# Kernel tuning notes

Measured on AMD Instinct MI355X. Metric: run time of the kernel, lower is better.

The kernel has to match this reference:

```python
import jax, jax.numpy as jnp
import numpy as np
from jax import lax

TWN_THRESHOLD_FACTOR = 0.05
BN_EPS = 1e-5


@jax.custom_vjp
def _ternary_quant(w, t):
    return (w > t).astype(w.dtype) - (w < -t).astype(w.dtype)

def _tq_fwd(w, t):
    mask = (w > t) | (w < -t)
    return _ternary_quant(w, t), mask

def _tq_bwd(mask, g):
    return (g * mask.astype(g.dtype), jnp.zeros((), g.dtype))

_ternary_quant.defvjp(_tq_fwd, _tq_bwd)


def quantize(w):
    # threshold is detached in the original (weight.detach().abs().max())
    t = TWN_THRESHOLD_FACTOR * jnp.max(jnp.abs(lax.stop_gradient(w)))
    return _ternary_quant(w, t)


def conv2d(x, w, b):
    # x: [N,C,H,W], w: [O,I,K,K], valid conv, stride 1
    y = lax.conv_general_dilated(x, w, (1, 1), 'VALID',
                                 dimension_numbers=('NCHW', 'OIHW', 'NCHW'))
    return y + b[None, :, None, None]


def maxpool2(x):
    return lax.reduce_window(x, -jnp.inf, lax.max,
                             (1, 1, 2, 2), (1, 1, 2, 2), 'VALID')


def bn2d(x, g, b):
    # training-mode batch norm over (N,H,W), biased variance
    m = jnp.mean(x, (0, 2, 3), keepdims=True)
    v = jnp.mean(jnp.square(x - m), (0, 2, 3), keepdims=True)
    return (x - m) * lax.rsqrt(v + BN_EPS) * g[None, :, None, None] + b[None, :, None, None]


def bn1d(x, g, b):
    m = jnp.mean(x, 0, keepdims=True)
    v = jnp.mean(jnp.square(x - m), 0, keepdims=True)
    return (x - m) * lax.rsqrt(v + BN_EPS) * g[None, :] + b[None, :]


def setup_inputs() -> dict:
    key = jax.random.key(0)
    ks = jax.random.split(key, 12)
    N = 4096
    inp = {
        'x': jax.random.normal(ks[0], (N, 1, 28, 28), jnp.float32),
        'w1': jax.random.normal(ks[1], (32, 1, 5, 5), jnp.float32) * 0.2,
        'b1': jnp.zeros((32,), jnp.float32),
        'g1': jnp.ones((32,), jnp.float32),
        'be1': jnp.zeros((32,), jnp.float32),
        'w2': jax.random.normal(ks[2], (64, 32, 5, 5), jnp.float32) * 0.05,
        'b2': jnp.zeros((64,), jnp.float32),
        'g2': jnp.ones((64,), jnp.float32),
        'be2': jnp.zeros((64,), jnp.float32),
        'wf1': jax.random.normal(ks[3], (512, 1024), jnp.float32) * 0.03,
        'bf1': jnp.zeros((512,), jnp.float32),
        'g3': jnp.ones((512,), jnp.float32),
        'be3': jnp.zeros((512,), jnp.float32),
        'wf2': jax.random.normal(ks[4], (10, 512), jnp.float32) * 0.04,
        'bf2': jnp.zeros((10,), jnp.float32),
    }
    return inp


def reference(x, w1, b1, g1, be1, w2, b2, g2, be2, wf1, bf1, g3, be3, wf2, bf2):
    h = jax.nn.relu(bn2d(conv2d(x, quantize(w1), b1), g1, be1))     # [N,32,24,24]
    h = maxpool2(h)                                                  # [N,32,12,12]
    h = jax.nn.relu(bn2d(conv2d(h, quantize(w2), b2), g2, be2))     # [N,64,8,8]
    h = maxpool2(h)                                                  # [N,64,4,4]
    h = h.reshape(h.shape[0], -1)                                    # [N,1024]
    h = jax.nn.relu(bn1d(h @ quantize(wf1).T + bf1, g3, be3))       # [N,512]
    return h @ quantize(wf2).T + bf2                                 # [N,10]
```

## Files before the change

### kernel.cpp

```cpp
#include <hip/hip_runtime.h>

#define TID ((int)threadIdx.x)
typedef unsigned short u16;
typedef short short8 __attribute__((ext_vector_type(8)));
typedef float f32x4 __attribute__((ext_vector_type(4)));

__device__ __forceinline__ u16 f2b(float f) {
    unsigned int x = __float_as_uint(f);
    return (u16)((x + 0x7fffu + ((x >> 16) & 1u)) >> 16);
}
__device__ __forceinline__ float b2f(u16 u) {
    return __uint_as_float(((unsigned int)u) << 16);
}
__device__ __forceinline__ unsigned int cvt_pk(float lo, float hi) {
    unsigned int r;
    asm("v_cvt_pk_bf16_f32 %0, %1, %2" : "=v"(r) : "v"(lo), "v"(hi));
    return r;
}

static constexpr size_t OFF_QW1   = 0;
static constexpr size_t OFF_QWF2  = 3200;
static constexpr size_t OFF_TMAX  = 23680;
static constexpr size_t OFF_SUM1C = 23808;
static constexpr size_t OFF_SSQ1C = 24832;
static constexpr size_t OFF_SUM2  = 25856, OFF_SSQ2 = 26112;
static constexpr size_t OFF_SUM3  = 26368, OFF_SSQ3 = 28416;
static constexpr size_t STATS_BEG = 23680, STATS_END = 30464;
static constexpr size_t OFF_QW2C  = 30720;
static constexpr size_t OFF_QWF1C = 133120;
static constexpr size_t OFF_Y1P   = 1181696;
static constexpr size_t OFF_H2P   = 38930432;
static constexpr size_t OFF_Y3    = 47319040;

__global__ __launch_bounds__(256) void absmax_k(const float* w1, const float* w2,
                                                const float* wf1, const float* wf2,
                                                unsigned int* tmaxbits) {
    int bid = blockIdx.x;
    int b, lb, nb; const float* src; long n;
    if (bid < 1)        { b = 0; src = w1;  n = 800;    lb = bid;       nb = 1;   }
    else if (bid < 9)   { b = 1; src = w2;  n = 51200;  lb = bid - 1;   nb = 8;   }
    else if (bid < 265) { b = 2; src = wf1; n = 524288; lb = bid - 9;   nb = 256; }
    else                { b = 3; src = wf2; n = 5120;   lb = bid - 265; nb = 1;   }
    float m = 0.f;
    for (long i = (long)lb * 256 + TID; i < n; i += (long)nb * 256)
        m = fmaxf(m, fabsf(src[i]));
    __shared__ float red[256];
    red[TID] = m; __syncthreads();
    for (int s = 128; s > 0; s >>= 1) {
        if (TID < s) red[TID] = fmaxf(red[TID], red[TID + s]);
        __syncthreads();
    }
    if (TID == 0) atomicMax(&tmaxbits[b], __float_as_uint(red[0]));
}

__global__ __launch_bounds__(256) void quant_all_k(const float* w1, const float* w2,
                                                   const float* wf1, const float* wf2,
                                                   float* qw1, u16* qw2c, u16* qwf1c,
                                                   float* qwf2, const unsigned int* tmax) {
    int bid = blockIdx.x;
    if (bid < 4) {
        int i = bid * 256 + TID; if (i >= 800) return;
        float t = 0.05f * __uint_as_float(tmax[0]);
        float v = w1[i];
        qw1[i] = (v > t) ? 1.f : ((v < -t) ? -1.f : 0.f);
    } else if (bid < 204) {
        int i = (bid - 4) * 256 + TID;
        float t = 0.05f * __uint_as_float(tmax[1]);
        int ic = i & 31, oc = (i >> 5) & 63, sh = i >> 11;
        float v = w2[(oc * 32 + ic) * 25 + sh];
        qw2c[i] = (v > t) ? (u16)0x3F80 : ((v < -t) ? (u16)0xBF80 : (u16)0);
    } else if (bid < 2252) {
        int i = (bid - 204) * 256 + TID;
        float t = 0.05f * __uint_as_float(tmax[2]);
        float v = wf1[i];
        qwf1c[i] = (v > t) ? (u16)0x3F80 : ((v < -t) ? (u16)0xBF80 : (u16)0);
    } else {
        int i = (bid - 2252) * 256 + TID;
        float t = 0.05f * __uint_as_float(tmax[3]);
        float v = wf2[i];
        qwf2[i] = (v > t) ? 1.f : ((v < -t) ? -1.f : 0.f);
    }
}

__global__ __launch_bounds__(256) void conv1_fused_k(const float* __restrict__ x,
                                                     const float* __restrict__ qw1,
                                                     u16* __restrict__ y1p,
                                                     float* sum1c, float* ssq1c) {
    __shared__ __align__(16) u16 xs[16 * 1096];
    int gid = blockIdx.x;
    int sg = gid >> 2, ph = (gid >> 1) & 1, pch = gid & 1;
    int l = TID & 63, w = TID >> 6;
    int lm = l & 15, q = l >> 4;

    #pragma unroll
    for (int i = 0; i < 9; i++) {
        int idx = TID + i * 256;
        if (idx < 2192) reinterpret_cast<uint4*>(xs)[idx] = make_uint4(0, 0, 0, 0);
    }

    short8 B1[2], B2[2];
    #pragma unroll
    for (int c = 0; c < 2; c++) {
        union { short8 s; u16 h[8]; } b1, b2;
        int ch = c * 16 + lm;
        #pragma unroll
        for (int j = 0; j < 8; j++) {
            float v1 = 0.f, v2 = 0.f;
            if (j < 5) {
                v1 = qw1[ch * 25 + q * 5 + j];
                v2 = qw1[ch * 25 + 20 + j];
            }
            b1.h[j] = f2b(v1);
            b2.h[j] = (q == 0) ? f2b(v2) : (u16)0;
        }
        B1[c] = b1.s; B2[c] = b2.s;
    }
    __syncthreads();

    #pragma unroll
    for (int k = 0; k < 7; k++) {
        int i = TID + k * 256;
        int smp = i / 112, rem = i % 112;
        int row = rem / 7, c4 = (rem % 7) * 4;
        float4 v = *reinterpret_cast<const float4*>(
            x + (size_t)(sg * 16 + smp) * 784 + (12 * ph + row) * 28 + c4);
        unsigned int r0 = cvt_pk(v.x, v.y), r1 = cvt_pk(v.z, v.w);
        uint2 pk; pk.x = r0; pk.y = r1;
        *reinterpret_cast<uint2*>(xs + smp * 1096 + row * 32 + c4) = pk;
        u16 h[4] = {(u16)r0, (u16)(r0 >> 16), (u16)r1, (u16)(r1 >> 16)};
        u16* b1p = xs + smp * 1096 + 548 + row * 32;
        #pragma unroll
        for (int e = 0; e < 4; e++) {
            int c = c4 + e;
            if (c >= 1) b1p[c - 1] = h[e];
        }
    }
    __syncthreads();

    float s0 = 0.f, s1 = 0.f, q0 = 0.f, q1 = 0.f;
    int laneoff = lm * 1096;
    #pragma unroll 1
    for (int e = 0; e < 9; e++) {
        int pp = w * 9 + e;
        int prl = pp / 6, pcl = pp - prl * 6;
        f32x4 pm0 = {-3.0e38f, -3.0e38f, -3.0e38f, -3.0e38f};
        f32x4 pm1 = pm0;
        #pragma unroll
        for (int dyx = 0; dyx < 4; dyx++) {
            int dy = dyx >> 1, dx = dyx & 1;
            int oyl = 2 * prl + dy;
            int ox = 2 * (pch * 6 + pcl) + dx;
            int r = ox & 1, cb = ox - r;
            const u16* p1 = xs + laneoff + r * 548 + (oyl + q) * 32 + cb;
            const u16* p2 = xs + laneoff + r * 548 + (oyl + 4) * 32 + cb;
            union { short8 s; unsigned int u[4]; } a1, a2;
            #pragma unroll
            for (int t = 0; t < 4; t++) {
                a1.u[t] = *reinterpret_cast<const unsigned int*>(p1 + 2 * t);
                a2.u[t] = *reinterpret_cast<const unsigned int*>(p2 + 2 * t);
            }
            f32x4 d0 = {0.f, 0.f, 0.f, 0.f};
            d0 = __builtin_amdgcn_mfma_f32_16x16x32_bf16(a1.s, B1[0], d0, 0, 0, 0);
            d0 = __builtin_amdgcn_mfma_f32_16x16x32_bf16(a2.s, B2[0], d0, 0, 0, 0);
            f32x4 d1 = {0.f, 0.f, 0.f, 0.f};
            d1 = __builtin_amdgcn_mfma_f32_16x16x32_bf16(a1.s, B1[1], d1, 0, 0, 0);
            d1 = __builtin_amdgcn_mfma_f32_16x16x32_bf16(a2.s, B2[1], d1, 0, 0, 0);
            #pragma unroll
            for (int i = 0; i < 4; i++) {
                float v = d0[i]; s0 += v; q0 = fmaf(v, v, q0);
                float u = d1[i]; s1 += u; q1 = fmaf(u, u, q1);
            }
            pm0 = __builtin_elementwise_max(pm0, d0);
            pm1 = __builtin_elementwise_max(pm1, d1);
        }
        int ppg = (ph * 6 + prl) * 12 + (pch * 6 + pcl);
        #pragma unroll
        for (int i = 0; i < 4; i++) {
            size_t nb = (size_t)(sg * 16 + 4 * q + i) * 4608 + ppg * 32;
            unsigned int r = cvt_pk(pm0[i], pm1[i]);
            y1p[nb + lm]      = (u16)r;
            y1p[nb + 16 + lm] = (u16)(r >> 16);
        }
    }
    s0 += __shfl_xor(s0, 16); s0 += __shfl_xor(s0, 32);
    s1 += __shfl_xor(s1, 16); s1 += __shfl_xor(s1, 32);
    q0 += __shfl_xor(q0, 16); q0 += __shfl_xor(q0, 32);
    q1 += __shfl_xor(q1, 16); q1 += __shfl_xor(q1, 32);
    if (l < 16) {
        int slot = (blockIdx.x & 7) * 32;
        atomicAdd(&sum1c[slot + l], s0);
        atomicAdd(&sum1c[slot + 16 + l], s1);
        atomicAdd(&ssq1c[slot + l], q0);
        atomicAdd(&ssq1c[slot + 16 + l], q1);
    }
}

__global__ __launch_bounds__(256, 2) void conv2_k(const u16* __restrict__ y1p,
                                                  const u16* __restrict__ qw2c,
                                                  u16* __restrict__ h2pre,
                                                  const float* sum1c, const float* ssq1c,
                                                  const float* g1, const float* be1,
                                                  float* sum, float* ssq) {
    __shared__ float4 hsm4[2352];
    __shared__ float scs[32], shs[32];
    char* hsraw = (char*)hsm4;
    int n0 = blockIdx.x * 8;
    int l = TID & 63, wv = TID >> 6;
    int oc0 = wv * 16;
    int lm = l & 15, sp = (l >> 3) & 1, ox = l & 7, bq = l >> 4;
    if (TID < 32) {
        float s = 0.f, q = 0.f;
        #pragma unroll
        for (int r = 0; r < 8; r++) { s += sum1c[r * 32 + TID]; q += ssq1c[r * 32 + TID]; }
        float m = s * (1.f / 2359296.f);
        float v = q * (1.f / 2359296.f) - m * m;
        float sc = g1[TID] / sqrtf(v + 1e-5f);
        scs[TID] = sc; shs[TID] = be1[TID] - m * sc;
    }
    __syncthreads();
    float scR[8], shR[8];
    {
        int b = TID & 3;
        #pragma unroll
        for (int j = 0; j < 8; j++) { scR[j] = scs[b * 8 + j]; shR[j] = shs[b * 8 + j]; }
    }
    short8 bw[25];
    #pragma unroll
    for (int sh = 0; sh < 25; sh++)
        bw[sh] = *reinterpret_cast<const short8*>(qw2c + ((size_t)sh * 64 + oc0 + lm) * 32 + bq * 8);
    int xy[5];
    #pragma unroll
    for (int kx = 0; kx < 5; kx++) {
        int xx = ox + kx;
        xy[kx] = sp * 9408 + xx * 64 + (((bq + (xx >> 1)) & 3) * 16);
    }
    float sacc = 0.f, s2acc = 0.f;
    {
        const uint4* src = reinterpret_cast<const uint4*>(y1p + (size_t)n0 * 4608);
        #pragma unroll
        for (int k = 0; k < 5; k++) {
            if (k < 4 || TID < 128) {
                int i = TID + k * 256;
                int smp = (i >= 576) ? 1 : 0;
                int j = i - smp * 576;
                int pix = j >> 2, b = j & 3;
                int y = pix / 12, xx = pix - y * 12;
                union { uint4 v; u16 u[8]; } in;
                in.v = src[i];
                float f[8];
                #pragma unroll
                for (int e = 0; e < 8; e++)
                    f[e] = fmaxf(fmaf(b2f(in.u[e]), scR[e], shR[e]), 0.f);
                uint4 o = make_uint4(cvt_pk(f[0], f[1]), cvt_pk(f[2], f[3]),
                                     cvt_pk(f[4], f[5]), cvt_pk(f[6], f[7]));
                *reinterpret_cast<uint4*>(hsraw + smp * 9408 + y * 784 + xx * 64 +
                                          (((b + (xx >> 1)) & 3) * 16)) = o;
            }
        }
    }
    #pragma unroll 1
    for (int t = 0; t < 4; t++) {
        __syncthreads();
        uint4 pf[5] = {};
        if (t < 3) {
            const uint4* src = reinterpret_cast<const uint4*>(y1p + (size_t)(n0 + 2 * (t + 1)) * 4608);
            #pragma unroll
            for (int k = 0; k < 5; k++)
                if (k < 4 || TID < 128) pf[k] = src[TID + k * 256];
        }
        const char* hb = hsraw + (t & 1) * 18816;
        f32x4 acc[8] = {{0.f,0.f,0.f,0.f},{0.f,0.f,0.f,0.f},{0.f,0.f,0.f,0.f},{0.f,0.f,0.f,0.f},
                        {0.f,0.f,0.f,0.f},{0.f,0.f,0.f,0.f},{0.f,0.f,0.f,0.f},{0.f,0.f,0.f,0.f}};
        #pragma unroll
        for (int R = 0; R <= 11; R++) {
            short8 a[5];
            #pragma unroll
            for (int kx = 0; kx < 5; kx++)
                a[kx] = *reinterpret_cast<const short8*>(hb + xy[kx] + R * 784);
            #pragma unroll
            for (int mt = 0; mt < 8; mt++) {
                int ky = R - mt;
                if (ky < 0 || ky > 4) continue;
                #pragma unroll
                for (int kx = 0; kx < 5; kx++)
                    acc[mt] = __builtin_amdgcn_mfma_f32_16x16x32_bf16(a[kx], bw[ky * 5 + kx], acc[mt], 0, 0, 0);
            }
        }
        int n = n0 + 2 * t + (bq >> 1);
        u16* hp = h2pre + (size_t)n * 1024 + (oc0 + lm) * 16 + (bq & 1) * 2;
        #pragma unroll
        for (int tp = 0; tp < 4; tp++) {
            f32x4 A0 = acc[2 * tp], A1 = acc[2 * tp + 1];
            float v0 = A0[0], v1 = A0[1], v2 = A0[2], v3 = A0[3];
            float u0 = A1[0], u1 = A1[1], u2 = A1[2], u3 = A1[3];
            sacc  += v0 + v1 + v2 + v3 + u0 + u1 + u2 + u3;
            s2acc += v0*v0 + v1*v1 + v2*v2 + v3*v3 + u0*u0 + u1*u1 + u2*u2 + u3*u3;
            float p0 = fmaxf(fmaxf(v0, v1), fmaxf(u0, u1));
            float p1 = fmaxf(fmaxf(v2, v3), fmaxf(u2, u3));
            *reinterpret_cast<unsigned int*>(hp + tp * 4) = cvt_pk(p0, p1);
        }
        if (t < 3) {
            char* dst = hsraw + ((t + 1) & 1) * 18816;
            #pragma unroll
            for (int k = 0; k < 5; k++) {
                if (k < 4 || TID < 128) {
                    int i = TID + k * 256;
                    int smp = (i >= 576) ? 1 : 0;
                    int j = i - smp * 576;
                    int pix = j >> 2, b = j & 3;
                    int y = pix / 12, xx = pix - y * 12;
                    union { uint4 v; u16 u[8]; } in;
                    in.v = pf[k];
                    float f[8];
                    #pragma unroll
                    for (int e = 0; e < 8; e++)
                        f[e] = fmaxf(fmaf(b2f(in.u[e]), scR[e], shR[e]), 0.f);
                    uint4 o = make_uint4(cvt_pk(f[0], f[1]), cvt_pk(f[2], f[3]),
                                         cvt_pk(f[4], f[5]), cvt_pk(f[6], f[7]));
                    *reinterpret_cast<uint4*>(dst + smp * 9408 + y * 784 + xx * 64 +
                                              (((b + (xx >> 1)) & 3) * 16)) = o;
                }
            }
        }
    }
    sacc  += __shfl_xor(sacc, 16);  sacc  += __shfl_xor(sacc, 32);
    s2acc += __shfl_xor(s2acc, 16); s2acc += __shfl_xor(s2acc, 32);
    if (l < 16) { atomicAdd(&sum[oc0 + l], sacc); atomicAdd(&ssq[oc0 + l], s2acc); }
}

__global__ __launch_bounds__(256) void fc1_k(const u16* __restrict__ h2pre,
                                             const u16* __restrict__ qwf1c,
                                             const float* sum2, const float* ssq2,
                                             const float* g2, const float* be2,
                                             float* __restrict__ y3T,
                                             float* sum3, float* ssq3) {
    __shared__ float4 Asm[2][576], Bsm[2][576];
    __shared__ float sc2s[64], sh2s[64];
    int m0 = blockIdx.x * 64, j0 = blockIdx.y * 64;
    int l = TID & 63, wv = TID >> 6;
    int lm = l & 15, q = l >> 4;
    int r0 = TID >> 3, c0 = TID & 7;
    if (TID < 64) {
        float m = sum2[TID] * (1.f / 262144.f);
        float v = ssq2[TID] * (1.f / 262144.f) - m * m;
        float s = g2[TID] / sqrtf(v + 1e-5f);
        sc2s[TID] = s; sh2s[TID] = be2[TID] - m * s;
    }
    __syncthreads();
    {
        u16* AsW = (u16*)Asm[0]; u16* BsW = (u16*)Bsm[0];
        int oc = (c0 * 8) >> 4;
        float sc = sc2s[oc], sh = sh2s[oc];
        #pragma unroll
        for (int i = 0; i < 2; i++) {
            int r = i * 32 + r0;
            union { float4 v; u16 h[8]; } in;
            in.v = *reinterpret_cast<const float4*>(h2pre + (size_t)(m0 + r) * 1024 + c0 * 8);
            float f[8];
            #pragma unroll
            for (int e = 0; e < 8; e++)
                f[e] = fmaxf(fmaf(b2f(in.h[e]), sc, sh), 0.f);
            uint4 o = make_uint4(cvt_pk(f[0], f[1]), cvt_pk(f[2], f[3]),
                                 cvt_pk(f[4], f[5]), cvt_pk(f[6], f[7]));
            *reinterpret_cast<uint4*>(AsW + r * 72 + c0 * 8) = o;
            *reinterpret_cast<float4*>(BsW + r * 72 + c0 * 8) =
                *reinterpret_cast<const float4*>(qwf1c + (size_t)(j0 + r) * 1024 + c0 * 8);
        }
    }
    f32x4 acc[4] = {{0.f,0.f,0.f,0.f},{0.f,0.f,0.f,0.f},{0.f,0.f,0.f,0.f},{0.f,0.f,0.f,0.f}};
    #pragma unroll 1
    for (int kc = 0; kc < 16; kc++) {
        __syncthreads();
        float4 pa0, pa1, pb0, pb1;
        if (kc < 15) {
            int kk = (kc + 1) * 64;
            pa0 = *reinterpret_cast<const float4*>(h2pre + (size_t)(m0 + r0) * 1024 + kk + c0 * 8);
            pa1 = *reinterpret_cast<const float4*>(h2pre + (size_t)(m0 + 32 + r0) * 1024 + kk + c0 * 8);
            pb0 = *reinterpret_cast<const float4*>(qwf1c + (size_t)(j0 + r0) * 1024 + kk + c0 * 8);
            pb1 = *reinterpret_cast<const float4*>(qwf1c + (size_t)(j0 + 32 + r0) * 1024 + kk + c0 * 8);
        }
        const u16* AsU = (const u16*)Asm[kc & 1];
        const u16* BsU = (const u16*)Bsm[kc & 1];
        #pragma unroll
        for (int half = 0; half < 2; half++) {
            short8 b = *reinterpret_cast<const short8*>(BsU + (wv * 16 + lm) * 72 + half * 32 + q * 8);
            #pragma unroll
            for (int mt = 0; mt < 4; mt++) {
                short8 a = *reinterpret_cast<const short8*>(AsU + (mt * 16 + lm) * 72 + half * 32 + q * 8);
                acc[mt] = __builtin_amdgcn_mfma_f32_16x16x32_bf16(a, b, acc[mt], 0, 0, 0);
            }
        }
        if (kc < 15) {
            int kk = (kc + 1) * 64;
            u16* AsW = (u16*)Asm[(kc + 1) & 1];
            u16* BsW = (u16*)Bsm[(kc + 1) & 1];
            int oc = (kk + c0 * 8) >> 4;
            float sc = sc2s[oc], sh = sh2s[oc];
            #pragma unroll
            for (int i = 0; i < 2; i++) {
                int r = i * 32 + r0;
                union { float4 v; u16 h[8]; } in;
                in.v = (i == 0) ? pa0 : pa1;
                float f[8];
                #pragma unroll
                for (int e = 0; e < 8; e++)
                    f[e] = fmaxf(fmaf(b2f(in.h[e]), sc, sh), 0.f);
                uint4 o = make_uint4(cvt_pk(f[0], f[1]), cvt_pk(f[2], f[3]),
                                     cvt_pk(f[4], f[5]), cvt_pk(f[6], f[7]));
                *reinterpret_cast<uint4*>(AsW + r * 72 + c0 * 8) = o;
                *reinterpret_cast<float4*>(BsW + r * 72 + c0 * 8) = (i == 0) ? pb0 : pb1;
            }
        }
    }
    float s = 0.f, s2 = 0.f;
    #pragma unroll
    for (int mt = 0; mt < 4; mt++) {
        *reinterpret_cast<f32x4*>(y3T + (size_t)(j0 + wv * 16 + lm) * 4096 + m0 + mt * 16 + q * 4) = acc[mt];
        #pragma unroll
        for (int i = 0; i < 4; i++) { float v = acc[mt][i]; s += v; s2 = fmaf(v, v, s2); }
    }
    s  += __shfl_xor(s, 16);  s  += __shfl_xor(s, 32);
    s2 += __shfl_xor(s2, 16); s2 += __shfl_xor(s2, 32);
    if (l < 16) {
        atomicAdd(&sum3[j0 + wv * 16 + l], s);
        atomicAdd(&ssq3[j0 + wv * 16 + l], s2);
    }
}

__global__ __launch_bounds__(256) void fc2_k(const float* __restrict__ y3T,
                                             const float* sum3, const float* ssq3,
                                             const float* g3, const float* be3,
                                             const float* __restrict__ qwf2,
                                             const float* bf2, float* __restrict__ out) {
    __shared__ float wlds[5120];
    __shared__ float part[15][160];
    __shared__ float sc3s[512], sh3s[512];
    for (int i = TID; i < 5120; i += 256) wlds[i] = qwf2[i];
    for (int k = TID; k < 512; k += 256) {
        float m = sum3[k] * (1.f / 4096.f);
        float v = ssq3[k] * (1.f / 4096.f) - m * m;
        float s = g3[k] / sqrtf(v + 1e-5f);
        sc3s[k] = s; sh3s[k] = be3[k] - m * s;
    }
    __syncthreads();
    int nl = TID & 15, ks = TID >> 4;
    int n = blockIdx.x * 16 + nl;
    float acc[10] = {};
    for (int k = ks * 32; k < ks * 32 + 32; k++) {
        float v = fmaxf(y3T[(size_t)k * 4096 + n] * sc3s[k] + sh3s[k], 0.f);
        #pragma unroll
        for (int o = 0; o < 10; o++) acc[o] = fmaf(v, wlds[o * 512 + k], acc[o]);
    }
    if (ks > 0) {
        #pragma unroll
        for (int o = 0; o < 10; o++) part[ks - 1][o * 16 + nl] = acc[o];
    }
    __syncthreads();
    if (ks == 0) {
        #pragma unroll
        for (int o = 0; o < 10; o++) {
            float r = acc[o] + bf2[o];
            #pragma unroll
            for (int j = 0; j < 15; j++) r += part[j][o * 16 + nl];
            out[n * 10 + o] = r;
        }
    }
}

extern "C" void kernel_launch(void* const* d_in, const int* in_sizes, int n_in,
                              void* d_out, int out_size, void* d_ws, size_t ws_size,
                              hipStream_t stream) {
    char* wsb = (char*)d_ws;
    const float* x   = (const float*)d_in[0];
    const float* w1  = (const float*)d_in[1];
    const float* g1  = (const float*)d_in[3];
    const float* be1 = (const float*)d_in[4];
    const float* w2  = (const float*)d_in[5];
    const float* g2  = (const float*)d_in[7];
    const float* be2 = (const float*)d_in[8];
    const float* wf1 = (const float*)d_in[9];
    const float* g3  = (const float*)d_in[11];
    const float* be3 = (const float*)d_in[12];
    const float* wf2 = (const float*)d_in[13];
    const float* bf2 = (const float*)d_in[14];
    float* out = (float*)d_out;

    unsigned int* tmax = (unsigned int*)(wsb + OFF_TMAX);
    float* qw1   = (float*)(wsb + OFF_QW1);
    float* qwf2  = (float*)(wsb + OFF_QWF2);
    u16*   qw2c  = (u16*)(wsb + OFF_QW2C);
    u16*   qwf1c = (u16*)(wsb + OFF_QWF1C);
    u16*   y1p   = (u16*)(wsb + OFF_Y1P);
    u16*   h2pre = (u16*)(wsb + OFF_H2P);
    float* y3    = (float*)(wsb + OFF_Y3);

    float* sum1c = (float*)(wsb + OFF_SUM1C); float* ssq1c = (float*)(wsb + OFF_SSQ1C);
    float* sum2  = (float*)(wsb + OFF_SUM2);  float* ssq2  = (float*)(wsb + OFF_SSQ2);
    float* sum3  = (float*)(wsb + OFF_SUM3);  float* ssq3  = (float*)(wsb + OFF_SSQ3);

    hipMemsetAsync(wsb + STATS_BEG, 0, STATS_END - STATS_BEG, stream);

    absmax_k<<<266, 256, 0, stream>>>(w1, w2, wf1, wf2, tmax);
    quant_all_k<<<2272, 256, 0, stream>>>(w1, w2, wf1, wf2, qw1, qw2c, qwf1c, qwf2, tmax);

    conv1_fused_k<<<1024, 256, 0, stream>>>(x, qw1, y1p, sum1c, ssq1c);
    conv2_k<<<512, 256, 0, stream>>>(y1p, qw2c, h2pre, sum1c, ssq1c, g1, be1, sum2, ssq2);
    fc1_k<<<dim3(64, 8), 256, 0, stream>>>(h2pre, qwf1c, sum2, ssq2, g2, be2, y3, sum3, ssq3);
    fc2_k<<<256, 256, 0, stream>>>(y3, sum3, ssq3, g3, be3, qwf2, bf2, out);
}
```

Baseline: 189.0 us.

## Stage all four conv2 sample pairs into shared memory upfront

The double-buffered prefetch loop in conv2 is replaced by a single load phase: the BN1+ReLU-transformed input for all 8 samples goes into a shared-memory buffer twice the size (about 75 KB), followed by one barrier and four back-to-back MFMA passes. This removes the per-iteration barriers and the register-held prefetch, cutting sync overhead and register pressure in the compute loop. In exchange, global loads no longer overlap MFMA work within a block, and the doubled LDS use may block two resident blocks per CU as requested by the launch bounds, lowering occupancy.

```diff
diff --git a/kernel.cpp b/kernel.cpp
--- a/kernel.cpp
+++ b/kernel.cpp
@@ -201,7 +201,7 @@
                                                   const float* sum1c, const float* ssq1c,
                                                   const float* g1, const float* be1,
                                                   float* sum, float* ssq) {
-    __shared__ float4 hsm4[2352];
+    __shared__ float4 hsm4[4704];
     __shared__ float scs[32], shs[32];
     char* hsraw = (char*)hsm4;
     int n0 = blockIdx.x * 8;
@@ -234,9 +234,10 @@
         int xx = ox + kx;
         xy[kx] = sp * 9408 + xx * 64 + (((bq + (xx >> 1)) & 3) * 16);
     }
-    float sacc = 0.f, s2acc = 0.f;
-    {
-        const uint4* src = reinterpret_cast<const uint4*>(y1p + (size_t)n0 * 4608);
+    #pragma unroll
+    for (int p = 0; p < 4; p++) {
+        const uint4* src = reinterpret_cast<const uint4*>(y1p + (size_t)(n0 + 2 * p) * 4608);
+        char* dst = hsraw + p * 18816;
         #pragma unroll
         for (int k = 0; k < 5; k++) {
             if (k < 4 || TID < 128) {
@@ -253,22 +254,15 @@
                     f[e] = fmaxf(fmaf(b2f(in.u[e]), scR[e], shR[e]), 0.f);
                 uint4 o = make_uint4(cvt_pk(f[0], f[1]), cvt_pk(f[2], f[3]),
                                      cvt_pk(f[4], f[5]), cvt_pk(f[6], f[7]));
-                *reinterpret_cast<uint4*>(hsraw + smp * 9408 + y * 784 + xx * 64 +
+                *reinterpret_cast<uint4*>(dst + smp * 9408 + y * 784 + xx * 64 +
                                           (((b + (xx >> 1)) & 3) * 16)) = o;
             }
         }
     }
-    #pragma unroll 1
-    for (int t = 0; t < 4; t++) {
-        __syncthreads();
-        uint4 pf[5] = {};
-        if (t < 3) {
-            const uint4* src = reinterpret_cast<const uint4*>(y1p + (size_t)(n0 + 2 * (t + 1)) * 4608);
-            #pragma unroll
-            for (int k = 0; k < 5; k++)
-                if (k < 4 || TID < 128) pf[k] = src[TID + k * 256];
-        }
-        const char* hb = hsraw + (t & 1) * 18816;
+    __syncthreads();
+    float sacc = 0.f, s2acc = 0.f;
+    for (int p = 0; p < 4; p++) {
+        const char* hb = hsraw + p * 18816;
         f32x4 acc[8] = {{0.f,0.f,0.f,0.f},{0.f,0.f,0.f,0.f},{0.f,0.f,0.f,0.f},{0.f,0.f,0.f,0.f},
                         {0.f,0.f,0.f,0.f},{0.f,0.f,0.f,0.f},{0.f,0.f,0.f,0.f},{0.f,0.f,0.f,0.f}};
         #pragma unroll
@@ -286,7 +280,7 @@
                     acc[mt] = __builtin_amdgcn_mfma_f32_16x16x32_bf16(a[kx], bw[ky * 5 + kx], acc[mt], 0, 0, 0);
             }
         }
-        int n = n0 + 2 * t + (bq >> 1);
+        int n = n0 + 2 * p + (bq >> 1);
         u16* hp = h2pre + (size_t)n * 1024 + (oc0 + lm) * 16 + (bq & 1) * 2;
         #pragma unroll
         for (int tp = 0; tp < 4; tp++) {
@@ -298,29 +292,6 @@
             float p0 = fmaxf(fmaxf(v0, v1), fmaxf(u0, u1));
             float p1 = fmaxf(fmaxf(v2, v3), fmaxf(u2, u3));
             *reinterpret_cast<unsigned int*>(hp + tp * 4) = cvt_pk(p0, p1);
-        }
-        if (t < 3) {
-            char* dst = hsraw + ((t + 1) & 1) * 18816;
-            #pragma unroll
-            for (int k = 0; k < 5; k++) {
-                if (k < 4 || TID < 128) {
-                    int i = TID + k * 256;
-                    int smp = (i >= 576) ? 1 : 0;
-                    int j = i - smp * 576;
-                    int pix = j >> 2, b = j & 3;
-                    int y = pix / 12, xx = pix - y * 12;
-                    union { uint4 v; u16 u[8]; } in;
-                    in.v = pf[k];
-                    float f[8];
-                    #pragma unroll
-                    for (int e = 0; e < 8; e++)
-                        f[e] = fmaxf(fmaf(b2f(in.u[e]), scR[e], shR[e]), 0.f);
-                    uint4 o = make_uint4(cvt_pk(f[0], f[1]), cvt_pk(f[2], f[3]),
-                                         cvt_pk(f[4], f[5]), cvt_pk(f[6], f[7]));
-                    *reinterpret_cast<uint4*>(dst + smp * 9408 + y * 784 + xx * 64 +
-                                              (((b + (xx >> 1)) & 3) * 16)) = o;
-                }
-            }
         }
     }
     sacc  += __shfl_xor(sacc, 16);  sacc  += __shfl_xor(sacc, 32);
```

New measurement: 191.1 us. Within noise of the previous version (+1.1%).
